# Performance work log

Hardware: AMD Instinct MI355X
Metric: run time of the kernel (lower is better)

## Reference

```python
import jax, jax.numpy as jnp
import numpy as np

N = 100000   # nodes
E = 1600000  # edges (before self loops)
G = 256      # graphs in batch
D_IN, H, D_OUT = 64, 64, 64
MLP_DIMS = [64, 128, 64, 1]
NEG_SLOPE = 0.2
BN_EPS = 1e-5


def setup_inputs() -> dict:
    key = jax.random.key(0)
    ks = jax.random.split(key, 40)
    inp = {}
    inp["x"] = jax.random.normal(ks[0], (N, D_IN), jnp.float32)
    src = jax.random.randint(ks[1], (E,), 0, N, dtype=jnp.int64)
    dst = jax.random.randint(ks[2], (E,), 0, N, dtype=jnp.int64)
    inp["edge_index"] = jnp.stack([src, dst])
    inp["batch"] = jnp.sort(jax.random.randint(ks[3], (N,), 0, G, dtype=jnp.int64))
    # GATv2 layer params (heads=1): lin_l, lin_r, attention vector, out bias
    dims = [(D_IN, H), (H, H), (H, D_OUT)]
    i = 4
    for l, (di, do) in enumerate(dims):
        s = 1.0 / np.sqrt(di)
        inp[f"Wl{l}"] = jax.random.normal(ks[i], (di, do), jnp.float32) * s; i += 1
        inp[f"bl{l}"] = jnp.zeros((do,), jnp.float32)
        inp[f"Wr{l}"] = jax.random.normal(ks[i], (di, do), jnp.float32) * s; i += 1
        inp[f"br{l}"] = jnp.zeros((do,), jnp.float32)
        inp[f"att{l}"] = jax.random.normal(ks[i], (do,), jnp.float32) * (1.0 / np.sqrt(do)); i += 1
        inp[f"b{l}"] = jnp.zeros((do,), jnp.float32)
    # MLP params (Linear + BatchNorm + ReLU, plain last layer)
    for l in range(len(MLP_DIMS) - 1):
        di, do = MLP_DIMS[l], MLP_DIMS[l + 1]
        s = 1.0 / np.sqrt(di)
        inp[f"mW{l}"] = jax.random.normal(ks[i], (di, do), jnp.float32) * s; i += 1
        inp[f"mb{l}"] = jnp.zeros((do,), jnp.float32)
        if l < len(MLP_DIMS) - 2:
            inp[f"g{l}"] = jnp.ones((do,), jnp.float32)
            inp[f"be{l}"] = jnp.zeros((do,), jnp.float32)
    return inp


def _gatv2(x, src, dst, Wl, bl, Wr, br, att, b):
    # GATv2Conv, heads=1: e_ij = att . LeakyReLU(Wl x_j + Wr x_i)
    xl = x @ Wl + bl            # messages from source nodes [N, C]
    xr = x @ Wr + br            # target-node term          [N, C]
    e = jax.nn.leaky_relu(xl[src] + xr[dst], NEG_SLOPE) @ att  # [E']
    # scatter-softmax over incoming edges of each dst node
    m = jax.ops.segment_max(e, dst, num_segments=N)
    w = jnp.exp(e - m[dst])
    denom = jax.ops.segment_sum(w, dst, num_segments=N)
    alpha = w / denom[dst]
    out = jax.ops.segment_sum(alpha[:, None] * xl[src], dst, num_segments=N)
    return out + b


def reference(x, edge_index, batch,
              Wl0, bl0, Wr0, br0, att0, b0,
              Wl1, bl1, Wr1, br1, att1, b1,
              Wl2, bl2, Wr2, br2, att2, b2,
              mW0, mb0, g0, be0, mW1, mb1, g1, be1, mW2, mb2):
    # add self loops (GATv2Conv default)
    loop = jnp.arange(N, dtype=edge_index.dtype)
    src = jnp.concatenate([edge_index[0], loop])
    dst = jnp.concatenate([edge_index[1], loop])
    # GAT stack: ReLU between layers, none after last
    h = jax.nn.relu(_gatv2(x, src, dst, Wl0, bl0, Wr0, br0, att0, b0))
    h = jax.nn.relu(_gatv2(h, src, dst, Wl1, bl1, Wr1, br1, att1, b1))
    h = _gatv2(h, src, dst, Wl2, bl2, Wr2, br2, att2, b2)
    # MLP: Linear -> BatchNorm (training stats) -> ReLU, plain last layer
    for W, bb, g, be in [(mW0, mb0, g0, be0), (mW1, mb1, g1, be1)]:
        h = h @ W + bb
        mu = jnp.mean(h, axis=0)
        var = jnp.var(h, axis=0)
        h = jax.nn.relu((h - mu) * jax.lax.rsqrt(var + BN_EPS) * g + be)
    h = h @ mW2 + mb2  # [N, 1]
    # global mean pool per graph
    sums = jax.ops.segment_sum(h, batch, num_segments=G)
    cnts = jax.ops.segment_sum(jnp.ones((N,), h.dtype), batch, num_segments=G)
    return sums / jnp.maximum(cnts, 1.0)[:, None]
```

## Files before the change

kernel.cpp:

```cpp
#include <hip/hip_runtime.h>
#include <hip/hip_bf16.h>
#include <hip/hip_fp16.h>
#include <math.h>


#define BSHIFT 9
#define BSIZE  512
#define STAGE_CAP 24576


__global__ __launch_bounds__(256) void k_bcount(const int* __restrict__ dstA,
                                                int* __restrict__ bcnt,
                                                int nE, int n) {
    __shared__ int h[512];
    int t = threadIdx.x;
    h[t] = 0; h[t + 256] = 0;
    __syncthreads();
    int tot = nE + n;
    for (int i = blockIdx.x * 256 + t; i < tot; i += gridDim.x * 256) {
        int d = (i < nE) ? dstA[i] : (i - nE);
        atomicAdd(&h[d >> BSHIFT], 1);
    }
    __syncthreads();
    if (h[t])       atomicAdd(&bcnt[t], h[t]);
    if (h[t + 256]) atomicAdd(&bcnt[t + 256], h[t + 256]);
}

__global__ __launch_bounds__(512) void k_bscan(const int* __restrict__ bcnt,
                                               int* __restrict__ bbase,
                                               int* __restrict__ bcur,
                                               int* __restrict__ rowptr,
                                               int nb, int n, int etot) {
    __shared__ int buf[512];
    int t = threadIdx.x;
    int v = (t < nb) ? bcnt[t] : 0;
    buf[t] = v;
    __syncthreads();
    for (int off = 1; off < 512; off <<= 1) {
        int x = (t >= off) ? buf[t - off] : 0;
        __syncthreads();
        buf[t] += x;
        __syncthreads();
    }
    if (t < nb) { int e = buf[t] - v; bbase[t] = e; bcur[t] = e; }
    if (t == nb) bbase[nb] = buf[nb - 1];
    if (t == 0) rowptr[n] = etot;
}

__global__ __launch_bounds__(256) void k_bpart(const int* __restrict__ srcA,
                                               const int* __restrict__ dstA,
                                               int* __restrict__ bcur,
                                               unsigned* __restrict__ ebuf,
                                               int nE, int n) {
    __shared__ int cnt[512];
    __shared__ int run[512];
    int t = threadIdx.x;
    cnt[t] = 0; cnt[t + 256] = 0;
    __syncthreads();
    int tot = nE + n;
    int chunk = (tot + gridDim.x - 1) / gridDim.x;
    int c0 = blockIdx.x * chunk;
    int c1 = min(c0 + chunk, tot);
    for (int i = c0 + t; i < c1; i += 256) {
        int d = (i < nE) ? dstA[i] : (i - nE);
        atomicAdd(&cnt[d >> BSHIFT], 1);
    }
    __syncthreads();
    int c = cnt[t];
    if (c) run[t] = atomicAdd(&bcur[t], c);
    int c2 = cnt[t + 256];
    if (c2) run[t + 256] = atomicAdd(&bcur[t + 256], c2);
    __syncthreads();
    cnt[t] = 0; cnt[t + 256] = 0;
    __syncthreads();
    for (int i = c0 + t; i < c1; i += 256) {
        int s, d;
        if (i < nE) { s = srcA[i]; d = dstA[i]; }
        else        { s = d = i - nE; }
        int b = d >> BSHIFT;
        int pos = run[b] + atomicAdd(&cnt[b], 1);
        ebuf[pos] = ((unsigned)s << BSHIFT) | (unsigned)(d & (BSIZE - 1));
    }
}

__global__ __launch_bounds__(512) void k_bfill(const unsigned* __restrict__ ebuf,
                                               const int* __restrict__ bbase,
                                               int* __restrict__ rowptr,
                                               int* __restrict__ csr,
                                               int n, int nb) {
    int b = blockIdx.x;
    int lo = bbase[b], hi = bbase[b + 1];
    int cnt = hi - lo;
    int node0 = b << BSHIFT;
    __shared__ int deg[512];
    __shared__ int sbuf[512];
    __shared__ int cur[512];
    __shared__ unsigned stage[STAGE_CAP];
    int t = threadIdx.x;
    deg[t] = 0;
    __syncthreads();
    bool st = (cnt <= STAGE_CAP);
    for (int i = lo + t; i < hi; i += 512) {
        unsigned e = ebuf[i];
        if (st) stage[i - lo] = e;
        atomicAdd(&deg[e & (BSIZE - 1)], 1);
    }
    __syncthreads();
    int d = deg[t];
    sbuf[t] = d;
    __syncthreads();
    for (int off = 1; off < 512; off <<= 1) {
        int x = (t >= off) ? sbuf[t - off] : 0;
        __syncthreads();
        sbuf[t] += x;
        __syncthreads();
    }
    int excl = sbuf[t] - d;
    if (node0 + t < n) rowptr[node0 + t] = lo + excl;
    cur[t] = excl;
    __syncthreads();
    for (int i = lo + t; i < hi; i += 512) {
        unsigned e = st ? stage[i - lo] : ebuf[i];
        int pos = atomicAdd(&cur[e & (BSIZE - 1)], 1);
        csr[lo + pos] = (int)(e >> BSHIFT);
    }
}


__global__ __launch_bounds__(256) void k_gat_gemm(
        const float* __restrict__ hin,
        const float* __restrict__ Wl, const float* __restrict__ bl,
        const float* __restrict__ Wr, const float* __restrict__ br,
        __half* __restrict__ xl, float* __restrict__ xr, int n) {
    __shared__ float rows[16][64];
    int tid = threadIdx.x;
    int col = tid & 63, rlane = tid >> 6;
    float wlr[64], wrr[64];
    #pragma unroll
    for (int k = 0; k < 64; ++k) {
        wlr[k] = Wl[k * 64 + col];
        wrr[k] = Wr[k * 64 + col];
    }
    float blc = bl[col], brc = br[col];
    int sr = tid >> 4, sc4 = (tid & 15) << 2;
    for (int r0 = blockIdx.x * 16; r0 < n; r0 += gridDim.x * 16) {
        int rr = r0 + sr;
        float4 v = make_float4(0.f, 0.f, 0.f, 0.f);
        if (rr < n) v = *reinterpret_cast<const float4*>(hin + (size_t)rr * 64 + sc4);
        *reinterpret_cast<float4*>(&rows[sr][sc4]) = v;
        __syncthreads();
        #pragma unroll
        for (int q = 0; q < 4; ++q) {
            int rI = rlane * 4 + q;
            int r = r0 + rI;
            float al = blc, ar = brc;
            const float4* rv = reinterpret_cast<const float4*>(rows[rI]);
            #pragma unroll
            for (int k4 = 0; k4 < 16; ++k4) {
                float4 h4 = rv[k4];
                al = fmaf(h4.x, wlr[k4 * 4 + 0], al); ar = fmaf(h4.x, wrr[k4 * 4 + 0], ar);
                al = fmaf(h4.y, wlr[k4 * 4 + 1], al); ar = fmaf(h4.y, wrr[k4 * 4 + 1], ar);
                al = fmaf(h4.z, wlr[k4 * 4 + 2], al); ar = fmaf(h4.z, wrr[k4 * 4 + 2], ar);
                al = fmaf(h4.w, wlr[k4 * 4 + 3], al); ar = fmaf(h4.w, wrr[k4 * 4 + 3], ar);
            }
            if (r < n) {
                xl[r * 64 + col] = __float2half_rn(al);
                xr[(size_t)r * 64 + col] = ar;
            }
        }
        __syncthreads();
    }
}


__global__ __launch_bounds__(256) void k_gat_edge(
        const __half* __restrict__ xl, const float* __restrict__ xr,
        const int* __restrict__ rowptr, const int* __restrict__ csr_src,
        const float* __restrict__ att, const float* __restrict__ bias,
        float* __restrict__ hout, int n, int do_relu) {
    int node = blockIdx.x * 4 + (threadIdx.x >> 6);
    if (node >= n) return;
    int lane = threadIdx.x & 63;
    int grp = lane >> 4, sub = lane & 15;
    int c0 = sub << 2;
    float4 attv = *reinterpret_cast<const float4*>(att + c0);
    float4 xrv  = *reinterpret_cast<const float4*>(xr + (size_t)node * 64 + c0);
    int beg = rowptr[node], end = rowptr[node + 1];
    float m = -INFINITY, s = 0.f;
    float acc0 = 0.f, acc1 = 0.f, acc2 = 0.f, acc3 = 0.f;
    for (int k0 = beg; k0 < end; k0 += 4) {
        int kk = k0 + grp;
        int idx = csr_src[kk < end ? kk : end - 1];
        uint2 raw = *reinterpret_cast<const uint2*>(xl + ((size_t)idx << 6) + c0);
        float2 f01 = __half22float2(*reinterpret_cast<__half2*>(&raw.x));
        float2 f23 = __half22float2(*reinterpret_cast<__half2*>(&raw.y));
        float v0 = f01.x, v1 = f01.y, v2 = f23.x, v3 = f23.y;
        float t0 = v0 + xrv.x; t0 = (t0 > 0.f) ? t0 : 0.2f * t0;
        float t1 = v1 + xrv.y; t1 = (t1 > 0.f) ? t1 : 0.2f * t1;
        float t2 = v2 + xrv.z; t2 = (t2 > 0.f) ? t2 : 0.2f * t2;
        float t3 = v3 + xrv.w; t3 = (t3 > 0.f) ? t3 : 0.2f * t3;
        float p = fmaf(t3, attv.w, fmaf(t2, attv.z, fmaf(t1, attv.y, t0 * attv.x)));
        p += __shfl_xor(p, 1);
        p += __shfl_xor(p, 2);
        p += __shfl_xor(p, 4);
        p += __shfl_xor(p, 8);
        float p0 = __shfl(p, sub);
        float p1 = __shfl(p, 16 + sub);
        float p2 = __shfl(p, 32 + sub);
        float p3 = __shfl(p, 48 + sub);
        int rem = end - k0;
        if (rem < 4) {
            if (rem <= 1) p1 = -INFINITY;
            if (rem <= 2) p2 = -INFINITY;
            if (rem <= 3) p3 = -INFINITY;
        }
        float mx = fmaxf(fmaxf(fmaxf(p0, p1), fmaxf(p2, p3)), m);
        float sc = __expf(m - mx);
        float w0 = __expf(p0 - mx), w1 = __expf(p1 - mx);
        float w2 = __expf(p2 - mx), w3 = __expf(p3 - mx);
        float wm = (grp < 2) ? ((grp == 0) ? w0 : w1) : ((grp == 2) ? w2 : w3);
        s = s * sc + ((w0 + w1) + (w2 + w3));
        acc0 = fmaf(wm, v0, acc0 * sc);
        acc1 = fmaf(wm, v1, acc1 * sc);
        acc2 = fmaf(wm, v2, acc2 * sc);
        acc3 = fmaf(wm, v3, acc3 * sc);
        m = mx;
    }
    acc0 += __shfl_xor(acc0, 16); acc0 += __shfl_xor(acc0, 32);
    acc1 += __shfl_xor(acc1, 16); acc1 += __shfl_xor(acc1, 32);
    acc2 += __shfl_xor(acc2, 16); acc2 += __shfl_xor(acc2, 32);
    acc3 += __shfl_xor(acc3, 16); acc3 += __shfl_xor(acc3, 32);
    float inv = 1.0f / s;
    float4 bv = *reinterpret_cast<const float4*>(bias + c0);
    float o0 = fmaf(acc0, inv, bv.x);
    float o1 = fmaf(acc1, inv, bv.y);
    float o2 = fmaf(acc2, inv, bv.z);
    float o3 = fmaf(acc3, inv, bv.w);
    if (do_relu) {
        o0 = fmaxf(o0, 0.f); o1 = fmaxf(o1, 0.f);
        o2 = fmaxf(o2, 0.f); o3 = fmaxf(o3, 0.f);
    }
    if (grp == 0) {
        *reinterpret_cast<float4*>(hout + (size_t)node * 64 + c0) =
            make_float4(o0, o1, o2, o3);
    }
}


template <int DIN, int DOUT, int BN_IN>
__global__ __launch_bounds__(256) void k_mlp_gemm(
        const float* __restrict__ hin, const float* __restrict__ W,
        const float* __restrict__ bias, float* __restrict__ z,
        float* __restrict__ stat_sum, float* __restrict__ stat_sq,
        const float* __restrict__ muI, const float* __restrict__ ivI,
        const float* __restrict__ gI, const float* __restrict__ beI,
        int n) {
    constexpr int COLS = DOUT / 64;
    constexpr int F4PT = DIN / 64;
    __shared__ float rows[16][DIN];
    __shared__ float red[256];
    int tid = threadIdx.x;
    int col = tid & 63, rlane = tid >> 6;
    float wreg[COLS][DIN];
    #pragma unroll
    for (int j = 0; j < COLS; ++j)
        #pragma unroll
        for (int k = 0; k < DIN; ++k)
            wreg[j][k] = W[k * DOUT + col + j * 64];
    float bc[COLS], ls[COLS], lq[COLS];
    #pragma unroll
    for (int j = 0; j < COLS; ++j) {
        bc[j] = bias[col + j * 64];
        ls[j] = 0.f; lq[j] = 0.f;
    }
    int srT[F4PT], scT[F4PT];
    float4 An[F4PT], Bn[F4PT];
    #pragma unroll
    for (int i = 0; i < F4PT; ++i) {
        int idx = tid + i * 256;
        srT[i] = idx / (DIN / 4);
        scT[i] = (idx % (DIN / 4)) * 4;
        if (BN_IN) {
            int c = scT[i];
            float4 iv4 = *reinterpret_cast<const float4*>(ivI + c);
            float4 g4  = *reinterpret_cast<const float4*>(gI + c);
            float4 mu4 = *reinterpret_cast<const float4*>(muI + c);
            float4 be4 = *reinterpret_cast<const float4*>(beI + c);
            An[i].x = iv4.x * g4.x; Bn[i].x = be4.x - mu4.x * An[i].x;
            An[i].y = iv4.y * g4.y; Bn[i].y = be4.y - mu4.y * An[i].y;
            An[i].z = iv4.z * g4.z; Bn[i].z = be4.z - mu4.z * An[i].z;
            An[i].w = iv4.w * g4.w; Bn[i].w = be4.w - mu4.w * An[i].w;
        }
    }
    for (int r0 = blockIdx.x * 16; r0 < n; r0 += gridDim.x * 16) {
        #pragma unroll
        for (int i = 0; i < F4PT; ++i) {
            int rr = r0 + srT[i];
            float4 v = make_float4(0.f, 0.f, 0.f, 0.f);
            if (rr < n) v = *reinterpret_cast<const float4*>(hin + (size_t)rr * DIN + scT[i]);
            if (BN_IN) {
                v.x = fmaxf(fmaf(v.x, An[i].x, Bn[i].x), 0.f);
                v.y = fmaxf(fmaf(v.y, An[i].y, Bn[i].y), 0.f);
                v.z = fmaxf(fmaf(v.z, An[i].z, Bn[i].z), 0.f);
                v.w = fmaxf(fmaf(v.w, An[i].w, Bn[i].w), 0.f);
            }
            *reinterpret_cast<float4*>(&rows[srT[i]][scT[i]]) = v;
        }
        __syncthreads();
        #pragma unroll
        for (int q = 0; q < 4; ++q) {
            int rI = rlane * 4 + q;
            int r = r0 + rI;
            float a[COLS];
            #pragma unroll
            for (int j = 0; j < COLS; ++j) a[j] = bc[j];
            const float4* rv = reinterpret_cast<const float4*>(rows[rI]);
            #pragma unroll
            for (int k4 = 0; k4 < DIN / 4; ++k4) {
                float4 h4 = rv[k4];
                #pragma unroll
                for (int j = 0; j < COLS; ++j) {
                    a[j] = fmaf(h4.x, wreg[j][k4 * 4 + 0], a[j]);
                    a[j] = fmaf(h4.y, wreg[j][k4 * 4 + 1], a[j]);
                    a[j] = fmaf(h4.z, wreg[j][k4 * 4 + 2], a[j]);
                    a[j] = fmaf(h4.w, wreg[j][k4 * 4 + 3], a[j]);
                }
            }
            if (r < n) {
                #pragma unroll
                for (int j = 0; j < COLS; ++j) {
                    z[(size_t)r * DOUT + col + j * 64] = a[j];
                    ls[j] += a[j];
                    lq[j] = fmaf(a[j], a[j], lq[j]);
                }
            }
        }
        __syncthreads();
    }
    #pragma unroll
    for (int j = 0; j < COLS; ++j) {
        __syncthreads();
        red[tid] = ls[j];
        __syncthreads();
        if (rlane == 0) {
            float t = red[col] + red[col + 64] + red[col + 128] + red[col + 192];
            atomicAdd(&stat_sum[col + j * 64], t);
        }
        __syncthreads();
        red[tid] = lq[j];
        __syncthreads();
        if (rlane == 0) {
            float t = red[col] + red[col + 64] + red[col + 128] + red[col + 192];
            atomicAdd(&stat_sq[col + j * 64], t);
        }
    }
}

__global__ void k_bn_fin(const float* __restrict__ ssum, const float* __restrict__ ssq,
                         float* __restrict__ mu, float* __restrict__ inv,
                         int n, int dout) {
    int c = threadIdx.x;
    if (c >= dout) return;
    float m = ssum[c] / (float)n;
    float v = ssq[c] / (float)n - m * m;
    mu[c]  = m;
    inv[c] = rsqrtf(fmaxf(v, 0.f) + 1e-5f);
}


__global__ __launch_bounds__(256) void k_pool_seg(
        const float* __restrict__ h2, const float* __restrict__ w2,
        const float* __restrict__ b2, const int* __restrict__ batch,
        const float* __restrict__ mu1, const float* __restrict__ iv1,
        const float* __restrict__ g1, const float* __restrict__ be1,
        float* __restrict__ out, int n) {
    int g = blockIdx.x;
    int tid = threadIdx.x;
    int lo = 0, hi = n;
    while (lo < hi) { int mid = (lo + hi) >> 1; if (batch[mid] < g) lo = mid + 1; else hi = mid; }
    int start = lo;
    hi = n;
    while (lo < hi) { int mid = (lo + hi) >> 1; if (batch[mid] < g + 1) lo = mid + 1; else hi = mid; }
    int end = lo;
    int cnt = end - start;

    int c = (tid << 2) & 63;
    float A0 = iv1[c] * g1[c],         B0 = be1[c] - mu1[c] * A0;
    float A1 = iv1[c + 1] * g1[c + 1], B1 = be1[c + 1] - mu1[c + 1] * A1;
    float A2 = iv1[c + 2] * g1[c + 2], B2 = be1[c + 2] - mu1[c + 2] * A2;
    float A3 = iv1[c + 3] * g1[c + 3], B3 = be1[c + 3] - mu1[c + 3] * A3;
    float wa = w2[c], wb = w2[c + 1], wc = w2[c + 2], wd = w2[c + 3];
    const float4* b4 = reinterpret_cast<const float4*>(h2 + (size_t)start * 64);
    long total4 = (long)cnt * 16;
    float acc = 0.f;
    for (long i = tid; i < total4; i += 256) {
        float4 v = b4[i];
        acc = fmaf(fmaxf(fmaf(v.x, A0, B0), 0.f), wa, acc);
        acc = fmaf(fmaxf(fmaf(v.y, A1, B1), 0.f), wb, acc);
        acc = fmaf(fmaxf(fmaf(v.z, A2, B2), 0.f), wc, acc);
        acc = fmaf(fmaxf(fmaf(v.w, A3, B3), 0.f), wd, acc);
    }
    __shared__ float red[256];
    red[tid] = acc; __syncthreads();
    for (int off = 128; off; off >>= 1) {
        if (tid < off) red[tid] += red[tid + off];
        __syncthreads();
    }
    if (tid == 0) out[g] = (cnt > 0) ? red[0] / (float)cnt + b2[0] : 0.f;
}


extern "C" void kernel_launch(void* const* d_in, const int* in_sizes, int n_in,
                              void* d_out, int out_size, void* d_ws, size_t ws_size,
                              hipStream_t stream) {
    const float* x     = (const float*)d_in[0];
    const int*   ei    = (const int*)d_in[1];
    const int*   batch = (const int*)d_in[2];

    const int N = in_sizes[0] / 64;
    const int E = in_sizes[1] / 2;
    const int G = out_size;
    const int Etot = E + N;
    const int NB = (N + BSIZE - 1) >> BSHIFT;

    const int* srcA = ei;
    const int* dstA = ei + E;

    const float* Wl[3]; const float* bl[3]; const float* Wr[3];
    const float* br[3]; const float* att[3]; const float* bb[3];
    for (int l = 0; l < 3; ++l) {
        int base = 3 + 6 * l;
        Wl[l]  = (const float*)d_in[base + 0];
        bl[l]  = (const float*)d_in[base + 1];
        Wr[l]  = (const float*)d_in[base + 2];
        br[l]  = (const float*)d_in[base + 3];
        att[l] = (const float*)d_in[base + 4];
        bb[l]  = (const float*)d_in[base + 5];
    }
    const float* mW0 = (const float*)d_in[21];
    const float* mb0 = (const float*)d_in[22];
    const float* g0  = (const float*)d_in[23];
    const float* be0 = (const float*)d_in[24];
    const float* mW1 = (const float*)d_in[25];
    const float* mb1 = (const float*)d_in[26];
    const float* g1  = (const float*)d_in[27];
    const float* be1 = (const float*)d_in[28];
    const float* mW2 = (const float*)d_in[29];
    const float* mb2 = (const float*)d_in[30];

    char* w = (char*)d_ws;
    auto alloc = [&](size_t bytes) -> void* {
        void* p = (void*)w;
        w += (bytes + 255) & ~(size_t)255;
        return p;
    };
    int*    rowptr = (int*)alloc((size_t)(N + 1) * 4);
    int*    csr    = (int*)alloc((size_t)Etot * 4);
    int*    bcnt   = (int*)alloc(512 * 4);
    int*    bbase  = (int*)alloc(520 * 4);
    int*    bcur   = (int*)alloc(512 * 4);
    __half* xl     = (__half*)alloc((size_t)N * 64 * 2);
    float*  xr     = (float*)alloc((size_t)N * 64 * 4);
    float*  zext   = (float*)alloc((size_t)N * 32 * 4);
    float*  h      = (float*)alloc((size_t)N * 64 * 4);
    float*  stats  = (float*)alloc(8 * 128 * 4);
    float*  z      = (float*)xl;
    unsigned* ebuf = (unsigned*)h;
    (void)zext;

    float* sum0 = stats;        float* sq0 = stats + 128;
    float* mu0  = stats + 256;  float* iv0 = stats + 384;
    float* sum1 = stats + 512;  float* sq1 = stats + 640;
    float* mu1  = stats + 768;  float* iv1 = stats + 896;

    hipMemsetAsync(bcnt, 0, 512 * 4, stream);
    k_bcount<<<256, 256, 0, stream>>>(dstA, bcnt, E, N);
    k_bscan<<<1, 512, 0, stream>>>(bcnt, bbase, bcur, rowptr, NB, N, Etot);
    k_bpart<<<256, 256, 0, stream>>>(srcA, dstA, bcur, ebuf, E, N);
    k_bfill<<<NB, 512, 0, stream>>>(ebuf, bbase, rowptr, csr, N, NB);

    int nodeBlocks = (N + 3) / 4;
    const float* hin = x;
    for (int l = 0; l < 3; ++l) {
        k_gat_gemm<<<2048, 256, 0, stream>>>(hin, Wl[l], bl[l], Wr[l], br[l],
                                             xl, xr, N);
        k_gat_edge<<<nodeBlocks, 256, 0, stream>>>(xl, xr, rowptr, csr,
                                                   att[l], bb[l], h, N,
                                                   (l < 2) ? 1 : 0);
        hin = h;
    }

    hipMemsetAsync(sum0, 0, 2 * 128 * 4, stream);
    k_mlp_gemm<64, 128, 0><<<2048, 256, 0, stream>>>(
        h, mW0, mb0, z, sum0, sq0, nullptr, nullptr, nullptr, nullptr, N);
    k_bn_fin<<<1, 128, 0, stream>>>(sum0, sq0, mu0, iv0, N, 128);

    hipMemsetAsync(sum1, 0, 2 * 128 * 4, stream);
    k_mlp_gemm<128, 64, 1><<<2048, 256, 0, stream>>>(
        z, mW1, mb1, h, sum1, sq1, mu0, iv0, g0, be0, N);
    k_bn_fin<<<1, 64, 0, stream>>>(sum1, sq1, mu1, iv1, N, 64);

    k_pool_seg<<<G, 256, 0, stream>>>(h, mW2, mb2, batch, mu1, iv1, g1, be1,
                                      (float*)d_out, N);
}
```

Baseline: 576.2 us.

## Move GEMM weights to shared memory and compute 4 columns per thread

```diff
diff --git a/kernel.cpp b/kernel.cpp
--- a/kernel.cpp
+++ b/kernel.cpp
@@ -132,43 +132,47 @@
         const float* __restrict__ Wl, const float* __restrict__ bl,
         const float* __restrict__ Wr, const float* __restrict__ br,
         __half* __restrict__ xl, float* __restrict__ xr, int n) {
-    __shared__ float rows[16][64];
+    __shared__ float sW[64 * 128];
     int tid = threadIdx.x;
-    int col = tid & 63, rlane = tid >> 6;
-    float wlr[64], wrr[64];
-    #pragma unroll
-    for (int k = 0; k < 64; ++k) {
-        wlr[k] = Wl[k * 64 + col];
-        wrr[k] = Wr[k * 64 + col];
-    }
-    float blc = bl[col], brc = br[col];
-    int sr = tid >> 4, sc4 = (tid & 15) << 2;
-    for (int r0 = blockIdx.x * 16; r0 < n; r0 += gridDim.x * 16) {
-        int rr = r0 + sr;
-        float4 v = make_float4(0.f, 0.f, 0.f, 0.f);
-        if (rr < n) v = *reinterpret_cast<const float4*>(hin + (size_t)rr * 64 + sc4);
-        *reinterpret_cast<float4*>(&rows[sr][sc4]) = v;
-        __syncthreads();
+    for (int i = tid; i < 64 * 128; i += 256) {
+        int k = i >> 7, c = i & 127;
+        sW[i] = (c < 64) ? Wl[k * 64 + c] : Wr[k * 64 + (c - 64)];
+    }
+    __syncthreads();
+    int cg = tid & 31;
+    int rl = tid >> 5;
+    int c0 = (cg & 15) * 4;
+    bool isL = (cg < 16);
+    float4 bias4 = isL ? *reinterpret_cast<const float4*>(bl + c0)
+                       : *reinterpret_cast<const float4*>(br + c0);
+    const float4* sW4 = reinterpret_cast<const float4*>(sW);
+    for (int r = blockIdx.x * 8 + rl; r < n; r += gridDim.x * 8) {
+        const float4* row4 = reinterpret_cast<const float4*>(hin + (size_t)r * 64);
+        float4 acc = bias4;
         #pragma unroll
-        for (int q = 0; q < 4; ++q) {
-            int rI = rlane * 4 + q;
-            int r = r0 + rI;
-            float al = blc, ar = brc;
-            const float4* rv = reinterpret_cast<const float4*>(rows[rI]);
-            #pragma unroll
-            for (int k4 = 0; k4 < 16; ++k4) {
-                float4 h4 = rv[k4];
-                al = fmaf(h4.x, wlr[k4 * 4 + 0], al); ar = fmaf(h4.x, wrr[k4 * 4 + 0], ar);
-                al = fmaf(h4.y, wlr[k4 * 4 + 1], al); ar = fmaf(h4.y, wrr[k4 * 4 + 1], ar);
-                al = fmaf(h4.z, wlr[k4 * 4 + 2], al); ar = fmaf(h4.z, wrr[k4 * 4 + 2], ar);
-                al = fmaf(h4.w, wlr[k4 * 4 + 3], al); ar = fmaf(h4.w, wrr[k4 * 4 + 3], ar);
-            }
-            if (r < n) {
-                xl[r * 64 + col] = __float2half_rn(al);
-                xr[(size_t)r * 64 + col] = ar;
-            }
-        }
-        __syncthreads();
+        for (int k4 = 0; k4 < 16; ++k4) {
+            float4 h4 = row4[k4];
+            float4 w0 = sW4[(k4 * 4 + 0) * 32 + cg];
+            float4 w1 = sW4[(k4 * 4 + 1) * 32 + cg];
+            float4 w2 = sW4[(k4 * 4 + 2) * 32 + cg];
+            float4 w3 = sW4[(k4 * 4 + 3) * 32 + cg];
+            acc.x = fmaf(h4.x, w0.x, acc.x); acc.y = fmaf(h4.x, w0.y, acc.y);
+            acc.z = fmaf(h4.x, w0.z, acc.z); acc.w = fmaf(h4.x, w0.w, acc.w);
+            acc.x = fmaf(h4.y, w1.x, acc.x); acc.y = fmaf(h4.y, w1.y, acc.y);
+            acc.z = fmaf(h4.y, w1.z, acc.z); acc.w = fmaf(h4.y, w1.w, acc.w);
+            acc.x = fmaf(h4.z, w2.x, acc.x); acc.y = fmaf(h4.z, w2.y, acc.y);
+            acc.z = fmaf(h4.z, w2.z, acc.z); acc.w = fmaf(h4.z, w2.w, acc.w);
+            acc.x = fmaf(h4.w, w3.x, acc.x); acc.y = fmaf(h4.w, w3.y, acc.y);
+            acc.z = fmaf(h4.w, w3.z, acc.z); acc.w = fmaf(h4.w, w3.w, acc.w);
+        }
+        if (isL) {
+            union { __half2 h2[2]; uint2 u; } pk;
+            pk.h2[0] = __floats2half2_rn(acc.x, acc.y);
+            pk.h2[1] = __floats2half2_rn(acc.z, acc.w);
+            *reinterpret_cast<uint2*>(xl + (size_t)r * 64 + c0) = pk.u;
+        } else {
+            *reinterpret_cast<float4*>(xr + (size_t)r * 64 + c0) = acc;
+        }
     }
 }
 
@@ -255,104 +259,79 @@
         const float* __restrict__ muI, const float* __restrict__ ivI,
         const float* __restrict__ gI, const float* __restrict__ beI,
         int n) {
-    constexpr int COLS = DOUT / 64;
-    constexpr int F4PT = DIN / 64;
-    __shared__ float rows[16][DIN];
-    __shared__ float red[256];
+    constexpr int CG  = DOUT / 4;
+    constexpr int RPB = 256 / CG;
+    __shared__ float sW[DIN * DOUT];
+    __shared__ float sA[128], sB[128];
+    __shared__ float4 red4[256];
     int tid = threadIdx.x;
-    int col = tid & 63, rlane = tid >> 6;
-    float wreg[COLS][DIN];
-    #pragma unroll
-    for (int j = 0; j < COLS; ++j)
-        #pragma unroll
-        for (int k = 0; k < DIN; ++k)
-            wreg[j][k] = W[k * DOUT + col + j * 64];
-    float bc[COLS], ls[COLS], lq[COLS];
-    #pragma unroll
-    for (int j = 0; j < COLS; ++j) {
-        bc[j] = bias[col + j * 64];
-        ls[j] = 0.f; lq[j] = 0.f;
-    }
-    int srT[F4PT], scT[F4PT];
-    float4 An[F4PT], Bn[F4PT];
-    #pragma unroll
-    for (int i = 0; i < F4PT; ++i) {
-        int idx = tid + i * 256;
-        srT[i] = idx / (DIN / 4);
-        scT[i] = (idx % (DIN / 4)) * 4;
-        if (BN_IN) {
-            int c = scT[i];
-            float4 iv4 = *reinterpret_cast<const float4*>(ivI + c);
-            float4 g4  = *reinterpret_cast<const float4*>(gI + c);
-            float4 mu4 = *reinterpret_cast<const float4*>(muI + c);
-            float4 be4 = *reinterpret_cast<const float4*>(beI + c);
-            An[i].x = iv4.x * g4.x; Bn[i].x = be4.x - mu4.x * An[i].x;
-            An[i].y = iv4.y * g4.y; Bn[i].y = be4.y - mu4.y * An[i].y;
-            An[i].z = iv4.z * g4.z; Bn[i].z = be4.z - mu4.z * An[i].z;
-            An[i].w = iv4.w * g4.w; Bn[i].w = be4.w - mu4.w * An[i].w;
-        }
-    }
-    for (int r0 = blockIdx.x * 16; r0 < n; r0 += gridDim.x * 16) {
-        #pragma unroll
-        for (int i = 0; i < F4PT; ++i) {
-            int rr = r0 + srT[i];
-            float4 v = make_float4(0.f, 0.f, 0.f, 0.f);
-            if (rr < n) v = *reinterpret_cast<const float4*>(hin + (size_t)rr * DIN + scT[i]);
+    for (int i = tid; i < DIN * DOUT; i += 256) sW[i] = W[i];
+    if (BN_IN && tid < DIN) {
+        float a = ivI[tid] * gI[tid];
+        sA[tid] = a;
+        sB[tid] = beI[tid] - muI[tid] * a;
+    }
+    __syncthreads();
+    int cg = tid % CG, rl = tid / CG;
+    int c0 = cg * 4;
+    float4 bias4 = *reinterpret_cast<const float4*>(bias + c0);
+    const float4* sW4 = reinterpret_cast<const float4*>(sW);
+    float4 ls = make_float4(0.f, 0.f, 0.f, 0.f);
+    float4 lq = make_float4(0.f, 0.f, 0.f, 0.f);
+    for (int r = blockIdx.x * RPB + rl; r < n; r += gridDim.x * RPB) {
+        const float4* row4 = reinterpret_cast<const float4*>(hin + (size_t)r * DIN);
+        float4 acc = bias4;
+        #pragma unroll 8
+        for (int k4 = 0; k4 < DIN / 4; ++k4) {
+            float4 h4 = row4[k4];
             if (BN_IN) {
-                v.x = fmaxf(fmaf(v.x, An[i].x, Bn[i].x), 0.f);
-                v.y = fmaxf(fmaf(v.y, An[i].y, Bn[i].y), 0.f);
-                v.z = fmaxf(fmaf(v.z, An[i].z, Bn[i].z), 0.f);
-                v.w = fmaxf(fmaf(v.w, An[i].w, Bn[i].w), 0.f);
+                int c = k4 * 4;
+                h4.x = fmaxf(fmaf(h4.x, sA[c],     sB[c]),     0.f);
+                h4.y = fmaxf(fmaf(h4.y, sA[c + 1], sB[c + 1]), 0.f);
+                h4.z = fmaxf(fmaf(h4.z, sA[c + 2], sB[c + 2]), 0.f);
+                h4.w = fmaxf(fmaf(h4.w, sA[c + 3], sB[c + 3]), 0.f);
             }
-            *reinterpret_cast<float4*>(&rows[srT[i]][scT[i]]) = v;
-        }
-        __syncthreads();
-        #pragma unroll
-        for (int q = 0; q < 4; ++q) {
-            int rI = rlane * 4 + q;
-            int r = r0 + rI;
-            float a[COLS];
-            #pragma unroll
-            for (int j = 0; j < COLS; ++j) a[j] = bc[j];
-            const float4* rv = reinterpret_cast<const float4*>(rows[rI]);
-            #pragma unroll
-            for (int k4 = 0; k4 < DIN / 4; ++k4) {
-                float4 h4 = rv[k4];
-                #pragma unroll
-                for (int j = 0; j < COLS; ++j) {
-                    a[j] = fmaf(h4.x, wreg[j][k4 * 4 + 0], a[j]);
-                    a[j] = fmaf(h4.y, wreg[j][k4 * 4 + 1], a[j]);
-                    a[j] = fmaf(h4.z, wreg[j][k4 * 4 + 2], a[j]);
-                    a[j] = fmaf(h4.w, wreg[j][k4 * 4 + 3], a[j]);
-                }
-            }
-            if (r < n) {
-                #pragma unroll
-                for (int j = 0; j < COLS; ++j) {
-                    z[(size_t)r * DOUT + col + j * 64] = a[j];
-                    ls[j] += a[j];
-                    lq[j] = fmaf(a[j], a[j], lq[j]);
-                }
-            }
-        }
-        __syncthreads();
-    }
-    #pragma unroll
-    for (int j = 0; j < COLS; ++j) {
-        __syncthreads();
-        red[tid] = ls[j];
-        __syncthreads();
-        if (rlane == 0) {
-            float t = red[col] + red[col + 64] + red[col + 128] + red[col + 192];
-            atomicAdd(&stat_sum[col + j * 64], t);
-        }
-        __syncthreads();
-        red[tid] = lq[j];
-        __syncthreads();
-        if (rlane == 0) {
-            float t = red[col] + red[col + 64] + red[col + 128] + red[col + 192];
-            atomicAdd(&stat_sq[col + j * 64], t);
-        }
+            float4 w0 = sW4[(k4 * 4 + 0) * CG + cg];
+            float4 w1 = sW4[(k4 * 4 + 1) * CG + cg];
+            float4 w2 = sW4[(k4 * 4 + 2) * CG + cg];
+            float4 w3 = sW4[(k4 * 4 + 3) * CG + cg];
+            acc.x = fmaf(h4.x, w0.x, acc.x); acc.y = fmaf(h4.x, w0.y, acc.y);
+            acc.z = fmaf(h4.x, w0.z, acc.z); acc.w = fmaf(h4.x, w0.w, acc.w);
+            acc.x = fmaf(h4.y, w1.x, acc.x); acc.y = fmaf(h4.y, w1.y, acc.y);
+            acc.z = fmaf(h4.y, w1.z, acc.z); acc.w = fmaf(h4.y, w1.w, acc.w);
+            acc.x = fmaf(h4.z, w2.x, acc.x); acc.y = fmaf(h4.z, w2.y, acc.y);
+            acc.z = fmaf(h4.z, w2.z, acc.z); acc.w = fmaf(h4.z, w2.w, acc.w);
+            acc.x = fmaf(h4.w, w3.x, acc.x); acc.y = fmaf(h4.w, w3.y, acc.y);
+            acc.z = fmaf(h4.w, w3.z, acc.z); acc.w = fmaf(h4.w, w3.w, acc.w);
+        }
+        *reinterpret_cast<float4*>(z + (size_t)r * DOUT + c0) = acc;
+        ls.x += acc.x; ls.y += acc.y; ls.z += acc.z; ls.w += acc.w;
+        lq.x = fmaf(acc.x, acc.x, lq.x); lq.y = fmaf(acc.y, acc.y, lq.y);
+        lq.z = fmaf(acc.z, acc.z, lq.z); lq.w = fmaf(acc.w, acc.w, lq.w);
+    }
+    __syncthreads();
+    red4[tid] = ls;
+    __syncthreads();
+    if (rl == 0) {
+        float4 t = red4[cg];
+        for (int g2 = 1; g2 < RPB; ++g2) {
+            float4 u = red4[g2 * CG + cg];
+            t.x += u.x; t.y += u.y; t.z += u.z; t.w += u.w;
+        }
+        atomicAdd(&stat_sum[c0],     t.x); atomicAdd(&stat_sum[c0 + 1], t.y);
+        atomicAdd(&stat_sum[c0 + 2], t.z); atomicAdd(&stat_sum[c0 + 3], t.w);
+    }
+    __syncthreads();
+    red4[tid] = lq;
+    __syncthreads();
+    if (rl == 0) {
+        float4 t = red4[cg];
+        for (int g2 = 1; g2 < RPB; ++g2) {
+            float4 u = red4[g2 * CG + cg];
+            t.x += u.x; t.y += u.y; t.z += u.z; t.w += u.w;
+        }
+        atomicAdd(&stat_sq[c0],     t.x); atomicAdd(&stat_sq[c0 + 1], t.y);
+        atomicAdd(&stat_sq[c0 + 2], t.z); atomicAdd(&stat_sq[c0 + 3], t.w);
     }
 }
 
```

Result: slower. 1.113 ms (+93.1%).

## Retile GAT linear GEMM into LDS weight panels and prefetch edge gathers

Applied to the files above, without the earlier changes.

```diff
diff --git a/kernel.cpp b/kernel.cpp
--- a/kernel.cpp
+++ b/kernel.cpp
@@ -132,43 +132,68 @@
         const float* __restrict__ Wl, const float* __restrict__ bl,
         const float* __restrict__ Wr, const float* __restrict__ br,
         __half* __restrict__ xl, float* __restrict__ xr, int n) {
-    __shared__ float rows[16][64];
+    __shared__ float sW[64 * 64];
     int tid = threadIdx.x;
-    int col = tid & 63, rlane = tid >> 6;
-    float wlr[64], wrr[64];
-    #pragma unroll
-    for (int k = 0; k < 64; ++k) {
-        wlr[k] = Wl[k * 64 + col];
-        wrr[k] = Wr[k * 64 + col];
-    }
-    float blc = bl[col], brc = br[col];
-    int sr = tid >> 4, sc4 = (tid & 15) << 2;
-    for (int r0 = blockIdx.x * 16; r0 < n; r0 += gridDim.x * 16) {
-        int rr = r0 + sr;
-        float4 v = make_float4(0.f, 0.f, 0.f, 0.f);
-        if (rr < n) v = *reinterpret_cast<const float4*>(hin + (size_t)rr * 64 + sc4);
-        *reinterpret_cast<float4*>(&rows[sr][sc4]) = v;
-        __syncthreads();
+    int bpp = gridDim.x >> 1;
+    int panel = (blockIdx.x >= bpp) ? 1 : 0;
+    int b2 = blockIdx.x - panel * bpp;
+    const float* Wsrc = panel ? Wr : Wl;
+    const float* bsrc = panel ? br : bl;
+    for (int i = tid; i < 64 * 64; i += 256) sW[i] = Wsrc[i];
+    __syncthreads();
+    int cg = tid & 15, rt = tid >> 4;
+    int c0 = cg * 4;
+    float4 bias4 = *reinterpret_cast<const float4*>(bsrc + c0);
+    const float4* sW4 = reinterpret_cast<const float4*>(sW);
+    for (int r0 = b2 * 64; r0 < n; r0 += bpp * 64) {
+        int rb = r0 + rt * 4;
+        const float4* rp[4];
         #pragma unroll
-        for (int q = 0; q < 4; ++q) {
-            int rI = rlane * 4 + q;
-            int r = r0 + rI;
-            float al = blc, ar = brc;
-            const float4* rv = reinterpret_cast<const float4*>(rows[rI]);
+        for (int i = 0; i < 4; ++i) {
+            int rc = rb + i; if (rc > n - 1) rc = n - 1;
+            rp[i] = reinterpret_cast<const float4*>(hin + (size_t)rc * 64);
+        }
+        float4 acc[4];
+        #pragma unroll
+        for (int i = 0; i < 4; ++i) acc[i] = bias4;
+        #pragma unroll 2
+        for (int k4 = 0; k4 < 16; ++k4) {
+            float4 w0 = sW4[(k4 * 4 + 0) * 16 + cg];
+            float4 w1 = sW4[(k4 * 4 + 1) * 16 + cg];
+            float4 w2 = sW4[(k4 * 4 + 2) * 16 + cg];
+            float4 w3 = sW4[(k4 * 4 + 3) * 16 + cg];
             #pragma unroll
-            for (int k4 = 0; k4 < 16; ++k4) {
-                float4 h4 = rv[k4];
-                al = fmaf(h4.x, wlr[k4 * 4 + 0], al); ar = fmaf(h4.x, wrr[k4 * 4 + 0], ar);
-                al = fmaf(h4.y, wlr[k4 * 4 + 1], al); ar = fmaf(h4.y, wrr[k4 * 4 + 1], ar);
-                al = fmaf(h4.z, wlr[k4 * 4 + 2], al); ar = fmaf(h4.z, wrr[k4 * 4 + 2], ar);
-                al = fmaf(h4.w, wlr[k4 * 4 + 3], al); ar = fmaf(h4.w, wrr[k4 * 4 + 3], ar);
+            for (int i = 0; i < 4; ++i) {
+                float4 h4 = rp[i][k4];
+                acc[i].x = fmaf(h4.x, w0.x, acc[i].x); acc[i].y = fmaf(h4.x, w0.y, acc[i].y);
+                acc[i].z = fmaf(h4.x, w0.z, acc[i].z); acc[i].w = fmaf(h4.x, w0.w, acc[i].w);
+                acc[i].x = fmaf(h4.y, w1.x, acc[i].x); acc[i].y = fmaf(h4.y, w1.y, acc[i].y);
+                acc[i].z = fmaf(h4.y, w1.z, acc[i].z); acc[i].w = fmaf(h4.y, w1.w, acc[i].w);
+                acc[i].x = fmaf(h4.z, w2.x, acc[i].x); acc[i].y = fmaf(h4.z, w2.y, acc[i].y);
+                acc[i].z = fmaf(h4.z, w2.z, acc[i].z); acc[i].w = fmaf(h4.z, w2.w, acc[i].w);
+                acc[i].x = fmaf(h4.w, w3.x, acc[i].x); acc[i].y = fmaf(h4.w, w3.y, acc[i].y);
+                acc[i].z = fmaf(h4.w, w3.z, acc[i].z); acc[i].w = fmaf(h4.w, w3.w, acc[i].w);
             }
-            if (r < n) {
-                xl[r * 64 + col] = __float2half_rn(al);
-                xr[(size_t)r * 64 + col] = ar;
+        }
+        if (panel == 0) {
+            #pragma unroll
+            for (int i = 0; i < 4; ++i) {
+                int r = rb + i;
+                if (r < n) {
+                    union { __half2 h2[2]; uint2 u; } pk;
+                    pk.h2[0] = __floats2half2_rn(acc[i].x, acc[i].y);
+                    pk.h2[1] = __floats2half2_rn(acc[i].z, acc[i].w);
+                    *reinterpret_cast<uint2*>(xl + (size_t)r * 64 + c0) = pk.u;
+                }
             }
-        }
-        __syncthreads();
+        } else {
+            #pragma unroll
+            for (int i = 0; i < 4; ++i) {
+                int r = rb + i;
+                if (r < n)
+                    *reinterpret_cast<float4*>(xr + (size_t)r * 64 + c0) = acc[i];
+            }
+        }
     }
 }
 
@@ -186,14 +211,20 @@
     float4 attv = *reinterpret_cast<const float4*>(att + c0);
     float4 xrv  = *reinterpret_cast<const float4*>(xr + (size_t)node * 64 + c0);
     int beg = rowptr[node], end = rowptr[node + 1];
+    int e1 = end - 1;
     float m = -INFINITY, s = 0.f;
     float acc0 = 0.f, acc1 = 0.f, acc2 = 0.f, acc3 = 0.f;
+    int kk = beg + grp; if (kk > e1) kk = e1;
+    int idx_c = csr_src[kk];
+    uint2 raw_c = *reinterpret_cast<const uint2*>(xl + ((size_t)idx_c << 6) + c0);
+    kk = beg + 4 + grp; if (kk > e1) kk = e1;
+    int idx_n = csr_src[kk];
     for (int k0 = beg; k0 < end; k0 += 4) {
-        int kk = k0 + grp;
-        int idx = csr_src[kk < end ? kk : end - 1];
-        uint2 raw = *reinterpret_cast<const uint2*>(xl + ((size_t)idx << 6) + c0);
-        float2 f01 = __half22float2(*reinterpret_cast<__half2*>(&raw.x));
-        float2 f23 = __half22float2(*reinterpret_cast<__half2*>(&raw.y));
+        uint2 raw_n = *reinterpret_cast<const uint2*>(xl + ((size_t)idx_n << 6) + c0);
+        int kk2 = k0 + 8 + grp; if (kk2 > e1) kk2 = e1;
+        int idx_n2 = csr_src[kk2];
+        float2 f01 = __half22float2(*reinterpret_cast<__half2*>(&raw_c.x));
+        float2 f23 = __half22float2(*reinterpret_cast<__half2*>(&raw_c.y));
         float v0 = f01.x, v1 = f01.y, v2 = f23.x, v3 = f23.y;
         float t0 = v0 + xrv.x; t0 = (t0 > 0.f) ? t0 : 0.2f * t0;
         float t1 = v1 + xrv.y; t1 = (t1 > 0.f) ? t1 : 0.2f * t1;
@@ -225,6 +256,8 @@
         acc2 = fmaf(wm, v2, acc2 * sc);
         acc3 = fmaf(wm, v3, acc3 * sc);
         m = mx;
+        raw_c = raw_n;
+        idx_n = idx_n2;
     }
     acc0 += __shfl_xor(acc0, 16); acc0 += __shfl_xor(acc0, 32);
     acc1 += __shfl_xor(acc1, 16); acc1 += __shfl_xor(acc1, 32);
@@ -480,10 +513,11 @@
     k_bfill<<<NB, 512, 0, stream>>>(ebuf, bbase, rowptr, csr, N, NB);
 
     int nodeBlocks = (N + 3) / 4;
+    int bppG = (N + 63) / 64;
     const float* hin = x;
     for (int l = 0; l < 3; ++l) {
-        k_gat_gemm<<<2048, 256, 0, stream>>>(hin, Wl[l], bl[l], Wr[l], br[l],
-                                             xl, xr, N);
+        k_gat_gemm<<<2 * bppG, 256, 0, stream>>>(hin, Wl[l], bl[l], Wr[l], br[l],
+                                                 xl, xr, N);
         k_gat_edge<<<nodeBlocks, 256, 0, stream>>>(xl, xr, rowptr, csr,
                                                    att[l], bb[l], h, N,
                                                    (l < 2) ? 1 : 0);
```

Result: slower. 597.8 us (+3.7%).
